# Kernel tuning notes

Measured on AMD Instinct MI355X. Metric: run time of the kernel, lower is better.

Reference implementation:

```python
import jax, jax.numpy as jnp
import numpy as np

B, T, IN = 512, 1024, 32
H, NL, DL, OUT = 128, 2, 256, 32


def _lstm_layer(xs, Wih, Whh, bih, bhh):
    # xs: [B, T, D]; Wih: [4H, D]; Whh: [4H, H]; biases: [4H]
    # PyTorch gate order: i, f, g, o
    x_gates = jnp.einsum('btd,gd->btg', xs, Wih) + bih + bhh  # [B,T,4H]

    def step(carry, xg):
        h, c = carry
        gates = xg + h @ Whh.T  # [B,4H]
        i, f, g, o = jnp.split(gates, 4, axis=-1)
        i = jax.nn.sigmoid(i)
        f = jax.nn.sigmoid(f)
        g = jnp.tanh(g)
        o = jax.nn.sigmoid(o)
        c = f * c + i * g
        h = o * jnp.tanh(c)
        return (h, c), h

    h0 = jnp.zeros((xs.shape[0], Whh.shape[1]), xs.dtype)
    c0 = jnp.zeros_like(h0)
    # scan over time axis
    (_, _), hs = jax.lax.scan(step, (h0, c0), jnp.swapaxes(x_gates, 0, 1))
    return jnp.swapaxes(hs, 0, 1)  # [B,T,H]


def setup_inputs() -> dict:
    key = jax.random.key(0)
    ks = jax.random.split(key, 16)
    s = 0.08  # ~1/sqrt(H)
    inp = {
        'x': jax.random.normal(ks[0], (B, T, IN), jnp.float32),
        'Wih0': jax.random.normal(ks[1], (4 * H, IN), jnp.float32) * s,
        'Whh0': jax.random.normal(ks[2], (4 * H, H), jnp.float32) * s,
        'bih0': jax.random.normal(ks[3], (4 * H,), jnp.float32) * s,
        'bhh0': jax.random.normal(ks[4], (4 * H,), jnp.float32) * s,
        'Wih1': jax.random.normal(ks[5], (4 * H, H), jnp.float32) * s,
        'Whh1': jax.random.normal(ks[6], (4 * H, H), jnp.float32) * s,
        'bih1': jax.random.normal(ks[7], (4 * H,), jnp.float32) * s,
        'bhh1': jax.random.normal(ks[8], (4 * H,), jnp.float32) * s,
        'W1': jax.random.normal(ks[9], (DL, H), jnp.float32) * s,
        'b1': jax.random.normal(ks[10], (DL,), jnp.float32) * s,
        'W2': jax.random.normal(ks[11], (OUT, DL), jnp.float32) * 0.06,
        'b2': jax.random.normal(ks[12], (OUT,), jnp.float32) * 0.06,
    }
    return inp


def reference(x, Wih0, Whh0, bih0, bhh0, Wih1, Whh1, bih1, bhh1, W1, b1, W2, b2):
    h = _lstm_layer(x, Wih0, Whh0, bih0, bhh0)
    h = _lstm_layer(h, Wih1, Whh1, bih1, bhh1)
    last = h[:, -1]  # [B,H]
    y = jax.nn.celu(last @ W1.T + b1)
    y = jax.nn.celu(y @ W2.T + b2)
    hidden_init = jnp.zeros((NL, x.shape[0], H), x.dtype)  # module returns its initial hidden
    return (y, hidden_init)
```

## Files before the change

### kernel.cpp

```cpp
#include <hip/hip_runtime.h>
#include <hip/hip_bf16.h>


#define DEV __device__ __forceinline__

typedef float f32x4 __attribute__((ext_vector_type(4)));
typedef short bf16x8 __attribute__((ext_vector_type(8)));
typedef unsigned short ushort_t;

DEV float sigm(float x) { return 1.f / (1.f + __expf(-x)); }
DEV float tanhfast(float x) { float e = __expf(2.f * x); return (e - 1.f) / (e + 1.f); }
DEV float celu1(float x) { return x > 0.f ? x : (__expf(x) - 1.f); }

DEV short f2bf(float f) {
    __hip_bfloat16 h = __float2bfloat16(f);
    return *reinterpret_cast<short*>(&h);
}

__global__ __launch_bounds__(256)
void cvt_bf16(const float* __restrict__ in, ushort_t* __restrict__ out, int n8)
{
    int i = blockIdx.x * 256 + threadIdx.x;
    if (i >= n8) return;
    const float4* p = (const float4*)(in + (size_t)i * 8);
    float4 a = p[0], b = p[1];
    bf16x8 v;
    v[0] = f2bf(a.x); v[1] = f2bf(a.y); v[2] = f2bf(a.z); v[3] = f2bf(a.w);
    v[4] = f2bf(b.x); v[5] = f2bf(b.y); v[6] = f2bf(b.z); v[7] = f2bf(b.w);
    *(bf16x8*)(out + (size_t)i * 8) = v;
}

template<int K, bool XMAP>
__global__ __launch_bounds__(256, 2)
void gemm_mfma(const ushort_t* __restrict__ A, const ushort_t* __restrict__ Wg,
               const float* __restrict__ bA, const float* __restrict__ bB,
               float* __restrict__ C, int t0, int TC)
{
    constexpr int SWB = K * 2;
    constexpr int SM  = (K == 32) ? 3 : 7;
    __shared__ char As[128 * SWB];
    __shared__ char Ws[128 * SWB];

    const int tid = threadIdx.x;
    const int r0 = blockIdx.x * 128;
    const int g0 = blockIdx.y * 128;
    const int lane = tid & 63, w = tid >> 6;
    const int lr = lane & 15, kg = lane >> 4;

    constexpr int UPR = SWB / 16;
    constexpr int NIT = 128 * UPR / 256;
#pragma unroll
    for (int e = 0; e < NIT; e++) {
        int idx = tid + e * 256;
        int row = idx / UPR;
        int kb  = (idx - row * UPR) * 16;
        int dst = row * SWB + (kb ^ ((row & SM) << 4));
        size_t src;
        int r = r0 + row;
        if (XMAP) {
            int b = r / TC, tt = r - b * TC;
            src = ((size_t)b * 1024 + (size_t)(t0 + tt)) * 32 + (size_t)(kb >> 1);
        } else {
            src = (size_t)r * K + (size_t)(kb >> 1);
        }
        *(bf16x8*)(As + dst) = *(const bf16x8*)(A + src);
        *(bf16x8*)(Ws + dst) = *(const bf16x8*)(Wg + (size_t)(g0 + row) * K + (size_t)(kb >> 1));
    }
    __syncthreads();

    f32x4 acc[2][8];
#pragma unroll
    for (int mi = 0; mi < 2; mi++)
#pragma unroll
        for (int n = 0; n < 8; n++) acc[mi][n] = (f32x4){0.f, 0.f, 0.f, 0.f};

    const int m0 = w * 32;
#pragma unroll
    for (int ks = 0; ks < K / 32; ks++) {
        const int kb = ks * 64 + kg * 16;
        const int ra0 = m0 + lr, ra1 = m0 + 16 + lr;
        bf16x8 a0 = *(const bf16x8*)(As + ra0 * SWB + (kb ^ ((ra0 & SM) << 4)));
        bf16x8 a1 = *(const bf16x8*)(As + ra1 * SWB + (kb ^ ((ra1 & SM) << 4)));
#pragma unroll
        for (int n = 0; n < 8; n++) {
            int wr = n * 16 + lr;
            bf16x8 bw = *(const bf16x8*)(Ws + wr * SWB + (kb ^ ((wr & SM) << 4)));
            acc[0][n] = __builtin_amdgcn_mfma_f32_16x16x32_bf16(a0, bw, acc[0][n], 0, 0, 0);
            acc[1][n] = __builtin_amdgcn_mfma_f32_16x16x32_bf16(a1, bw, acc[1][n], 0, 0, 0);
        }
    }

#pragma unroll
    for (int n = 0; n < 8; n++) {
        int g = g0 + n * 16 + lr;
        float bias = bA[g] + bB[g];
#pragma unroll
        for (int mi = 0; mi < 2; mi++) {
            int rrow = r0 + m0 + mi * 16 + kg * 4;
#pragma unroll
            for (int rr = 0; rr < 4; rr++)
                C[(size_t)(rrow + rr) * 512 + g] = acc[mi][n][rr] + bias;
        }
    }
}

template<int WRITE_H>
DEV void scan_body(const float* __restrict__ xg, const ushort_t* __restrict__ whh,
                   float* __restrict__ hs, float* __restrict__ cs,
                   ushort_t* __restrict__ hout, int TC, int blk)
{
    __shared__ short h_lds[16 * 128];
    __shared__ float pre[4 * 4 * 128];

    const int t    = threadIdx.x;
    const int lane = t & 63;
    const int w    = t >> 6;
    const int b0   = blk * 4;
    const int um   = t >> 7;
    const int uch  = t & 127;
    const int lr   = lane & 15, kg = lane >> 4;

    bf16x8 Wf[4][4];
#pragma unroll
    for (int q = 0; q < 4; q++)
#pragma unroll
        for (int kt = 0; kt < 4; kt++)
            Wf[q][kt] = *(const bf16x8*)(whh + (size_t)(q * 128 + w * 16 + lr) * 128
                                              + kt * 32 + kg * 8);
    asm volatile("" : "+v"(Wf[0][0]), "+v"(Wf[0][1]), "+v"(Wf[0][2]), "+v"(Wf[0][3]),
                      "+v"(Wf[1][0]), "+v"(Wf[1][1]), "+v"(Wf[1][2]), "+v"(Wf[1][3]),
                      "+v"(Wf[2][0]), "+v"(Wf[2][1]), "+v"(Wf[2][2]), "+v"(Wf[2][3]),
                      "+v"(Wf[3][0]), "+v"(Wf[3][1]), "+v"(Wf[3][2]), "+v"(Wf[3][3]));

    float c_reg  = cs[(size_t)(b0 + um) * 128 + uch];
    float h_keep = hs[(size_t)(b0 + um) * 128 + uch];
    *(short*)((char*)h_lds + um * 256 + ((uch * 2) ^ (um << 4))) = f2bf(h_keep);
    if (t < 384)
        *(unsigned long long*)((char*)h_lds + 4 * 256 + t * 8) = 0ull;
    __syncthreads();

    const int abase = lr * 256;
    const int aswz  = (lr & 7) << 4;
    const int akoff = kg * 16;

    for (int tt = 0; tt < TC; tt++) {
        const size_t xr = ((size_t)(b0 + um) * TC + tt) * 512 + uch;
        float xv0 = xg[xr];
        float xv1 = xg[xr + 128];
        float xv2 = xg[xr + 256];
        float xv3 = xg[xr + 384];

        bf16x8 Af[4];
#pragma unroll
        for (int kt = 0; kt < 4; kt++)
            Af[kt] = *(const bf16x8*)((const char*)h_lds + abase + ((kt * 64 + akoff) ^ aswz));

        f32x4 acc[4];
#pragma unroll
        for (int q = 0; q < 4; q++) {
            f32x4 a = {0.f, 0.f, 0.f, 0.f};
#pragma unroll
            for (int kt = 0; kt < 4; kt++)
                a = __builtin_amdgcn_mfma_f32_16x16x32_bf16(Af[kt], Wf[q][kt], a, 0, 0, 0);
            acc[q] = a;
        }

        if (kg == 0) {
            const int chw = w * 16 + lr;
#pragma unroll
            for (int q = 0; q < 4; q++)
#pragma unroll
                for (int r = 0; r < 4; r++)
                    pre[q * 512 + r * 128 + chw] = acc[q][r];
        }
        __syncthreads();

        float pi = pre[0 * 512 + um * 128 + uch] + xv0;
        float pf = pre[1 * 512 + um * 128 + uch] + xv1;
        float pg = pre[2 * 512 + um * 128 + uch] + xv2;
        float po = pre[3 * 512 + um * 128 + uch] + xv3;
        float iv = sigm(pi), fv = sigm(pf), gv = tanhfast(pg), ov = sigm(po);
        c_reg = fv * c_reg + iv * gv;
        float hv = ov * tanhfast(c_reg);
        h_keep = hv;
        short hb = f2bf(hv);
        *(short*)((char*)h_lds + um * 256 + ((uch * 2) ^ (um << 4))) = hb;
        if (WRITE_H)
            hout[((size_t)(b0 + um) * TC + tt) * 128 + uch] = (ushort_t)hb;
        __syncthreads();
    }

    hs[(size_t)(b0 + um) * 128 + uch] = h_keep;
    cs[(size_t)(b0 + um) * 128 + uch] = c_reg;
}

template<int WRITE_H>
__global__ __launch_bounds__(512, 2)
void lstm_scan(const float* __restrict__ xg, const ushort_t* __restrict__ whh,
               float* __restrict__ hs, float* __restrict__ cs,
               ushort_t* __restrict__ hout, int TC)
{
    scan_body<WRITE_H>(xg, whh, hs, cs, hout, TC, blockIdx.x);
}

__global__ __launch_bounds__(512, 2)
void lstm_scan_dual(const float* __restrict__ xg0, const ushort_t* __restrict__ whh0,
                    float* __restrict__ h0s, float* __restrict__ c0s,
                    ushort_t* __restrict__ hout,
                    const float* __restrict__ xg1, const ushort_t* __restrict__ whh1,
                    float* __restrict__ h1s, float* __restrict__ c1s, int TC)
{
    if (blockIdx.x < 128)
        scan_body<1>(xg0, whh0, h0s, c0s, hout, TC, blockIdx.x);
    else
        scan_body<0>(xg1, whh1, h1s, c1s, nullptr, TC, blockIdx.x - 128);
}

__global__ __launch_bounds__(256, 2)
void head_k(const float* __restrict__ h1s, const float* __restrict__ W1,
            const float* __restrict__ b1, const float* __restrict__ W2,
            const float* __restrict__ b2, float* __restrict__ out)
{
    __shared__ float hrow[128];
    __shared__ float y1[256];
    const int b = blockIdx.x;
    const int tid = threadIdx.x;
    if (tid < 128) hrow[tid] = h1s[(size_t)b * 128 + tid];
    __syncthreads();
    {
        float acc = b1[tid];
        const float4* wp = (const float4*)(W1 + (size_t)tid * 128);
        const float4* hp = (const float4*)hrow;
#pragma unroll 8
        for (int q = 0; q < 32; q++) {
            float4 wv = wp[q]; float4 hv = hp[q];
            acc += wv.x * hv.x + wv.y * hv.y + wv.z * hv.z + wv.w * hv.w;
        }
        y1[tid] = celu1(acc);
    }
    __syncthreads();
    if (tid < 32) {
        float acc = b2[tid];
        const float4* wp = (const float4*)(W2 + (size_t)tid * 256);
        const float4* yp = (const float4*)y1;
#pragma unroll 8
        for (int q = 0; q < 64; q++) {
            float4 wv = wp[q]; float4 yv = yp[q];
            acc += wv.x * yv.x + wv.y * yv.y + wv.z * yv.z + wv.w * yv.w;
        }
        out[(size_t)b * 32 + tid] = celu1(acc);
    }
}

extern "C" void kernel_launch(void* const* d_in, const int* in_sizes, int n_in,
                              void* d_out, int out_size, void* d_ws, size_t ws_size,
                              hipStream_t stream)
{
    const float* x    = (const float*)d_in[0];
    const float* Wih0 = (const float*)d_in[1];
    const float* Whh0 = (const float*)d_in[2];
    const float* bih0 = (const float*)d_in[3];
    const float* bhh0 = (const float*)d_in[4];
    const float* Wih1 = (const float*)d_in[5];
    const float* Whh1 = (const float*)d_in[6];
    const float* bih1 = (const float*)d_in[7];
    const float* bhh1 = (const float*)d_in[8];
    const float* W1   = (const float*)d_in[9];
    const float* b1   = (const float*)d_in[10];
    const float* W2   = (const float*)d_in[11];
    const float* b2   = (const float*)d_in[12];
    float* out = (float*)d_out;

    const size_t XN = 512ull * 1024 * 32;
    int TC = 128;
    while (TC > 8) {
        size_t need = (size_t)(2 * TC) * 512 * 512 * 4
                    + 4ull * 512 * 128 * 4
                    + ((size_t)512 * TC * 128 + XN + 512 * 32 + 3ull * 512 * 128) * 2;
        if (need <= ws_size) break;
        TC >>= 1;
    }

    float* xg0 = (float*)d_ws;
    float* xg1 = xg0 + (size_t)512 * TC * 512;
    float* st  = xg1 + (size_t)512 * TC * 512;
    float* h0s = st;
    float* c0s = st + 512 * 128;
    float* h1s = st + 2 * 512 * 128;
    float* c1s = st + 3 * 512 * 128;
    ushort_t* h0c  = (ushort_t*)(st + 4ull * 512 * 128);
    ushort_t* xbf  = h0c + (size_t)512 * TC * 128;
    ushort_t* wih0 = xbf + XN;
    ushort_t* wih1 = wih0 + 512 * 32;
    ushort_t* whh0 = wih1 + 512 * 128;
    ushort_t* whh1 = whh0 + 512 * 128;

    hipMemsetAsync(st, 0, (size_t)4 * 512 * 128 * 4, stream);
    hipMemsetAsync(out + 16384, 0, (size_t)131072 * 4, stream);

    cvt_bf16<<<(unsigned)(XN / 8 / 256), 256, 0, stream>>>(x, xbf, (int)(XN / 8));
    cvt_bf16<<<8,   256, 0, stream>>>(Wih0, wih0, 512 * 32 / 8);
    cvt_bf16<<<32,  256, 0, stream>>>(Wih1, wih1, 512 * 128 / 8);
    cvt_bf16<<<32,  256, 0, stream>>>(Whh0, whh0, 512 * 128 / 8);
    cvt_bf16<<<32,  256, 0, stream>>>(Whh1, whh1, 512 * 128 / 8);

    const int NC = 1024 / TC;
    dim3 ggrid((unsigned)(512 * TC / 128), 4);

    gemm_mfma<32, true ><<<ggrid, 256, 0, stream>>>(xbf, wih0, bih0, bhh0, xg0, 0, TC);
    lstm_scan<1><<<128, 512, 0, stream>>>(xg0, whh0, h0s, c0s, h0c, TC);
    for (int c = 1; c < NC; c++) {
        gemm_mfma<128, false><<<ggrid, 256, 0, stream>>>(h0c, wih1, bih1, bhh1, xg1, 0, TC);
        gemm_mfma<32,  true ><<<ggrid, 256, 0, stream>>>(xbf, wih0, bih0, bhh0, xg0, c * TC, TC);
        lstm_scan_dual<<<256, 512, 0, stream>>>(xg0, whh0, h0s, c0s, h0c,
                                                xg1, whh1, h1s, c1s, TC);
    }
    gemm_mfma<128, false><<<ggrid, 256, 0, stream>>>(h0c, wih1, bih1, bhh1, xg1, 0, TC);
    lstm_scan<0><<<128, 512, 0, stream>>>(xg1, whh1, h1s, c1s, nullptr, TC);

    head_k<<<512, 256, 0, stream>>>(h1s, W1, b1, W2, b2, out);
}
```

Measured before the change: 1.643 ms.

## Fuse bf16 conversion into GEMMs, store gate preacts in fp16, restructure scan step

Drops the separate fp32-to-bf16 conversion kernels and converts x and weights inside the GEMM tile loads and the scan prologue. The two per-chunk input-projection GEMMs are merged into one launch that selects its path by grid z. Precomputed gate inputs are stored as fp16 instead of fp32, halving that traffic. The scan step now applies gate activations directly from MFMA accumulators in the lanes that hold them, uses a double-buffered h tile in LDS so each step needs one barrier instead of two, and prefetches the next step's gate inputs into registers. The trade-offs are fp16 precision loss on gate preactivations, only 16 of 64 lanes per wave doing the elementwise work, and repeated conversion of x and weights on every GEMM tile.

```diff
diff --git a/kernel.cpp b/kernel.cpp
--- a/kernel.cpp
+++ b/kernel.cpp
@@ -1,5 +1,6 @@
 #include <hip/hip_runtime.h>
 #include <hip/hip_bf16.h>
+#include <hip/hip_fp16.h>
 
 
 #define DEV __device__ __forceinline__
@@ -16,34 +17,29 @@
     __hip_bfloat16 h = __float2bfloat16(f);
     return *reinterpret_cast<short*>(&h);
 }
-
-__global__ __launch_bounds__(256)
-void cvt_bf16(const float* __restrict__ in, ushort_t* __restrict__ out, int n8)
-{
-    int i = blockIdx.x * 256 + threadIdx.x;
-    if (i >= n8) return;
-    const float4* p = (const float4*)(in + (size_t)i * 8);
-    float4 a = p[0], b = p[1];
-    bf16x8 v;
-    v[0] = f2bf(a.x); v[1] = f2bf(a.y); v[2] = f2bf(a.z); v[3] = f2bf(a.w);
-    v[4] = f2bf(b.x); v[5] = f2bf(b.y); v[6] = f2bf(b.z); v[7] = f2bf(b.w);
-    *(bf16x8*)(out + (size_t)i * 8) = v;
+DEV ushort_t f2h(float f) {
+    __half h = __float2half(f);
+    return *reinterpret_cast<ushort_t*>(&h);
+}
+DEV float h2f(ushort_t u) {
+    __half h;
+    *reinterpret_cast<ushort_t*>(&h) = u;
+    return __half2float(h);
 }
 
 template<int K, bool XMAP>
-__global__ __launch_bounds__(256, 2)
-void gemm_mfma(const ushort_t* __restrict__ A, const ushort_t* __restrict__ Wg,
-               const float* __restrict__ bA, const float* __restrict__ bB,
-               float* __restrict__ C, int t0, int TC)
+DEV void gemm_body(char* lds, const void* Av, const float* __restrict__ Wg,
+                   const float* __restrict__ bA, const float* __restrict__ bB,
+                   ushort_t* __restrict__ C, int t0, int TC, int bx, int by)
 {
     constexpr int SWB = K * 2;
     constexpr int SM  = (K == 32) ? 3 : 7;
-    __shared__ char As[128 * SWB];
-    __shared__ char Ws[128 * SWB];
+    char* As = lds;
+    char* Ws = lds + 128 * SWB;
 
     const int tid = threadIdx.x;
-    const int r0 = blockIdx.x * 128;
-    const int g0 = blockIdx.y * 128;
+    const int r0 = bx * 128;
+    const int g0 = by * 128;
     const int lane = tid & 63, w = tid >> 6;
     const int lr = lane & 15, kg = lane >> 4;
 
@@ -55,16 +51,29 @@
         int row = idx / UPR;
         int kb  = (idx - row * UPR) * 16;
         int dst = row * SWB + (kb ^ ((row & SM) << 4));
-        size_t src;
-        int r = r0 + row;
+        int ke  = kb >> 1;
+        bf16x8 av;
         if (XMAP) {
+            const float* A = (const float*)Av;
+            int r = r0 + row;
             int b = r / TC, tt = r - b * TC;
-            src = ((size_t)b * 1024 + (size_t)(t0 + tt)) * 32 + (size_t)(kb >> 1);
+            const float* p = A + ((size_t)b * 1024 + (size_t)(t0 + tt)) * 32 + ke;
+            float4 f0 = *(const float4*)p, f1 = *(const float4*)(p + 4);
+            av[0] = f2bf(f0.x); av[1] = f2bf(f0.y); av[2] = f2bf(f0.z); av[3] = f2bf(f0.w);
+            av[4] = f2bf(f1.x); av[5] = f2bf(f1.y); av[6] = f2bf(f1.z); av[7] = f2bf(f1.w);
         } else {
-            src = (size_t)r * K + (size_t)(kb >> 1);
-        }
-        *(bf16x8*)(As + dst) = *(const bf16x8*)(A + src);
-        *(bf16x8*)(Ws + dst) = *(const bf16x8*)(Wg + (size_t)(g0 + row) * K + (size_t)(kb >> 1));
+            const ushort_t* A = (const ushort_t*)Av;
+            av = *(const bf16x8*)(A + (size_t)(r0 + row) * K + ke);
+        }
+        *(bf16x8*)(As + dst) = av;
+        {
+            const float* p = Wg + (size_t)(g0 + row) * K + ke;
+            float4 f0 = *(const float4*)p, f1 = *(const float4*)(p + 4);
+            bf16x8 wv;
+            wv[0] = f2bf(f0.x); wv[1] = f2bf(f0.y); wv[2] = f2bf(f0.z); wv[3] = f2bf(f0.w);
+            wv[4] = f2bf(f1.x); wv[5] = f2bf(f1.y); wv[6] = f2bf(f1.z); wv[7] = f2bf(f1.w);
+            *(bf16x8*)(Ws + dst) = wv;
+        }
     }
     __syncthreads();
 
@@ -99,62 +108,97 @@
             int rrow = r0 + m0 + mi * 16 + kg * 4;
 #pragma unroll
             for (int rr = 0; rr < 4; rr++)
-                C[(size_t)(rrow + rr) * 512 + g] = acc[mi][n][rr] + bias;
-        }
-    }
+                C[(size_t)(rrow + rr) * 512 + g] = f2h(acc[mi][n][rr] + bias);
+        }
+    }
+}
+
+template<int MODE>
+__global__ __launch_bounds__(256, 2)
+void gemm_pair(const float* __restrict__ x, const float* __restrict__ wih0,
+               const float* __restrict__ bih0, const float* __restrict__ bhh0,
+               ushort_t* __restrict__ xg0, int t0,
+               const ushort_t* __restrict__ h0c, const float* __restrict__ wih1,
+               const float* __restrict__ bih1, const float* __restrict__ bhh1,
+               ushort_t* __restrict__ xg1, int TC)
+{
+    __shared__ char lds[65536];
+    const int path = (MODE == 0) ? (int)blockIdx.z : ((MODE == 1) ? 0 : 1);
+    if (path == 0)
+        gemm_body<32,  true >(lds, x,   wih0, bih0, bhh0, xg0, t0, TC,
+                              blockIdx.x, blockIdx.y);
+    else
+        gemm_body<128, false>(lds, h0c, wih1, bih1, bhh1, xg1, 0, TC,
+                              blockIdx.x, blockIdx.y);
 }
 
 template<int WRITE_H>
-DEV void scan_body(const float* __restrict__ xg, const ushort_t* __restrict__ whh,
+DEV void scan_body(const ushort_t* __restrict__ xg, const float* __restrict__ whh,
                    float* __restrict__ hs, float* __restrict__ cs,
                    ushort_t* __restrict__ hout, int TC, int blk)
 {
-    __shared__ short h_lds[16 * 128];
-    __shared__ float pre[4 * 4 * 128];
+    __shared__ char hb[2][1024];
 
     const int t    = threadIdx.x;
     const int lane = t & 63;
     const int w    = t >> 6;
     const int b0   = blk * 4;
-    const int um   = t >> 7;
-    const int uch  = t & 127;
     const int lr   = lane & 15, kg = lane >> 4;
+    const int ch   = w * 16 + lr;
+    const int arow = lr & 3;
 
     bf16x8 Wf[4][4];
 #pragma unroll
     for (int q = 0; q < 4; q++)
 #pragma unroll
+        for (int kt = 0; kt < 4; kt++) {
+            const float* p = whh + (size_t)(q * 128 + ch) * 128 + kt * 32 + kg * 8;
+            bf16x8 v;
+#pragma unroll
+            for (int j = 0; j < 8; j++) v[j] = f2bf(p[j]);
+            Wf[q][kt] = v;
+        }
+
+    float cst[4] = {0.f, 0.f, 0.f, 0.f};
+    float hk[4]  = {0.f, 0.f, 0.f, 0.f};
+    if (lane < 16) {
+#pragma unroll
+        for (int r = 0; r < 4; r++) {
+            hk[r]  = hs[(size_t)(b0 + r) * 128 + ch];
+            cst[r] = cs[(size_t)(b0 + r) * 128 + ch];
+            *(short*)(&hb[0][0] + r * 256 + ((ch * 2) ^ (r << 6))) = f2bf(hk[r]);
+        }
+    }
+    __syncthreads();
+
+    ushort_t xpA[16], xpB[16];
+    if (lane < 16) {
+#pragma unroll
+        for (int r = 0; r < 4; r++)
+#pragma unroll
+            for (int q = 0; q < 4; q++)
+                xpA[r * 4 + q] = xg[(size_t)(b0 + r) * TC * 512 + q * 128 + ch];
+    }
+
+    auto step = [&](int tt, int rb, ushort_t (&xu)[16], ushort_t (&xl)[16], bool pre) {
+        asm volatile("" : "+v"(Wf[0][0]), "+v"(Wf[0][1]), "+v"(Wf[0][2]), "+v"(Wf[0][3]),
+                          "+v"(Wf[1][0]), "+v"(Wf[1][1]), "+v"(Wf[1][2]), "+v"(Wf[1][3]),
+                          "+v"(Wf[2][0]), "+v"(Wf[2][1]), "+v"(Wf[2][2]), "+v"(Wf[2][3]),
+                          "+v"(Wf[3][0]), "+v"(Wf[3][1]), "+v"(Wf[3][2]), "+v"(Wf[3][3]));
+        const char* hbase = hb[rb];
+        bf16x8 Af[4];
+#pragma unroll
         for (int kt = 0; kt < 4; kt++)
-            Wf[q][kt] = *(const bf16x8*)(whh + (size_t)(q * 128 + w * 16 + lr) * 128
-                                              + kt * 32 + kg * 8);
-    asm volatile("" : "+v"(Wf[0][0]), "+v"(Wf[0][1]), "+v"(Wf[0][2]), "+v"(Wf[0][3]),
-                      "+v"(Wf[1][0]), "+v"(Wf[1][1]), "+v"(Wf[1][2]), "+v"(Wf[1][3]),
-                      "+v"(Wf[2][0]), "+v"(Wf[2][1]), "+v"(Wf[2][2]), "+v"(Wf[2][3]),
-                      "+v"(Wf[3][0]), "+v"(Wf[3][1]), "+v"(Wf[3][2]), "+v"(Wf[3][3]));
-
-    float c_reg  = cs[(size_t)(b0 + um) * 128 + uch];
-    float h_keep = hs[(size_t)(b0 + um) * 128 + uch];
-    *(short*)((char*)h_lds + um * 256 + ((uch * 2) ^ (um << 4))) = f2bf(h_keep);
-    if (t < 384)
-        *(unsigned long long*)((char*)h_lds + 4 * 256 + t * 8) = 0ull;
-    __syncthreads();
-
-    const int abase = lr * 256;
-    const int aswz  = (lr & 7) << 4;
-    const int akoff = kg * 16;
-
-    for (int tt = 0; tt < TC; tt++) {
-        const size_t xr = ((size_t)(b0 + um) * TC + tt) * 512 + uch;
-        float xv0 = xg[xr];
-        float xv1 = xg[xr + 128];
-        float xv2 = xg[xr + 256];
-        float xv3 = xg[xr + 384];
-
-        bf16x8 Af[4];
-#pragma unroll
-        for (int kt = 0; kt < 4; kt++)
-            Af[kt] = *(const bf16x8*)((const char*)h_lds + abase + ((kt * 64 + akoff) ^ aswz));
-
+            Af[kt] = *(const bf16x8*)(hbase + arow * 256
+                                      + ((kt * 64 + kg * 16) ^ (arow << 6)));
+        if (pre && lane < 16) {
+#pragma unroll
+            for (int r = 0; r < 4; r++)
+#pragma unroll
+                for (int q = 0; q < 4; q++)
+                    xl[r * 4 + q] = xg[((size_t)(b0 + r) * TC + (tt + 1)) * 512
+                                       + q * 128 + ch];
+        }
         f32x4 acc[4];
 #pragma unroll
         for (int q = 0; q < 4; q++) {
@@ -164,39 +208,44 @@
                 a = __builtin_amdgcn_mfma_f32_16x16x32_bf16(Af[kt], Wf[q][kt], a, 0, 0, 0);
             acc[q] = a;
         }
-
-        if (kg == 0) {
-            const int chw = w * 16 + lr;
-#pragma unroll
-            for (int q = 0; q < 4; q++)
-#pragma unroll
-                for (int r = 0; r < 4; r++)
-                    pre[q * 512 + r * 128 + chw] = acc[q][r];
+        if (lane < 16) {
+            char* hw = hb[rb ^ 1];
+#pragma unroll
+            for (int r = 0; r < 4; r++) {
+                float pi = acc[0][r] + h2f(xu[r * 4 + 0]);
+                float pf = acc[1][r] + h2f(xu[r * 4 + 1]);
+                float pg = acc[2][r] + h2f(xu[r * 4 + 2]);
+                float po = acc[3][r] + h2f(xu[r * 4 + 3]);
+                float iv = sigm(pi), fv = sigm(pf), gv = tanhfast(pg), ov = sigm(po);
+                cst[r] = fv * cst[r] + iv * gv;
+                float hv = ov * tanhfast(cst[r]);
+                hk[r] = hv;
+                short hb16 = f2bf(hv);
+                *(short*)(hw + r * 256 + ((ch * 2) ^ (r << 6))) = hb16;
+                if (WRITE_H)
+                    hout[((size_t)(b0 + r) * TC + tt) * 128 + ch] = (ushort_t)hb16;
+            }
         }
         __syncthreads();
-
-        float pi = pre[0 * 512 + um * 128 + uch] + xv0;
-        float pf = pre[1 * 512 + um * 128 + uch] + xv1;
-        float pg = pre[2 * 512 + um * 128 + uch] + xv2;
-        float po = pre[3 * 512 + um * 128 + uch] + xv3;
-        float iv = sigm(pi), fv = sigm(pf), gv = tanhfast(pg), ov = sigm(po);
-        c_reg = fv * c_reg + iv * gv;
-        float hv = ov * tanhfast(c_reg);
-        h_keep = hv;
-        short hb = f2bf(hv);
-        *(short*)((char*)h_lds + um * 256 + ((uch * 2) ^ (um << 4))) = hb;
-        if (WRITE_H)
-            hout[((size_t)(b0 + um) * TC + tt) * 128 + uch] = (ushort_t)hb;
-        __syncthreads();
-    }
-
-    hs[(size_t)(b0 + um) * 128 + uch] = h_keep;
-    cs[(size_t)(b0 + um) * 128 + uch] = c_reg;
+    };
+
+    for (int tt = 0; tt < TC; tt += 2) {
+        step(tt,     0, xpA, xpB, true);
+        step(tt + 1, 1, xpB, xpA, (tt + 2) < TC);
+    }
+
+    if (lane < 16) {
+#pragma unroll
+        for (int r = 0; r < 4; r++) {
+            hs[(size_t)(b0 + r) * 128 + ch] = hk[r];
+            cs[(size_t)(b0 + r) * 128 + ch] = cst[r];
+        }
+    }
 }
 
 template<int WRITE_H>
 __global__ __launch_bounds__(512, 2)
-void lstm_scan(const float* __restrict__ xg, const ushort_t* __restrict__ whh,
+void lstm_scan(const ushort_t* __restrict__ xg, const float* __restrict__ whh,
                float* __restrict__ hs, float* __restrict__ cs,
                ushort_t* __restrict__ hout, int TC)
 {
@@ -204,10 +253,10 @@
 }
 
 __global__ __launch_bounds__(512, 2)
-void lstm_scan_dual(const float* __restrict__ xg0, const ushort_t* __restrict__ whh0,
+void lstm_scan_dual(const ushort_t* __restrict__ xg0, const float* __restrict__ whh0,
                     float* __restrict__ h0s, float* __restrict__ c0s,
                     ushort_t* __restrict__ hout,
-                    const float* __restrict__ xg1, const ushort_t* __restrict__ whh1,
+                    const ushort_t* __restrict__ xg1, const float* __restrict__ whh1,
                     float* __restrict__ h1s, float* __restrict__ c1s, int TC)
 {
     if (blockIdx.x < 128)
@@ -271,52 +320,42 @@
     const float* b2   = (const float*)d_in[12];
     float* out = (float*)d_out;
 
-    const size_t XN = 512ull * 1024 * 32;
     int TC = 128;
     while (TC > 8) {
-        size_t need = (size_t)(2 * TC) * 512 * 512 * 4
-                    + 4ull * 512 * 128 * 4
-                    + ((size_t)512 * TC * 128 + XN + 512 * 32 + 3ull * 512 * 128) * 2;
+        size_t need = 2ull * 512 * TC * 512 * 2 + (size_t)512 * TC * 128 * 2
+                    + 4ull * 512 * 128 * 4;
         if (need <= ws_size) break;
         TC >>= 1;
     }
 
-    float* xg0 = (float*)d_ws;
-    float* xg1 = xg0 + (size_t)512 * TC * 512;
-    float* st  = xg1 + (size_t)512 * TC * 512;
+    ushort_t* xg0 = (ushort_t*)d_ws;
+    ushort_t* xg1 = xg0 + (size_t)512 * TC * 512;
+    ushort_t* h0c = xg1 + (size_t)512 * TC * 512;
+    float* st  = (float*)(h0c + (size_t)512 * TC * 128);
     float* h0s = st;
     float* c0s = st + 512 * 128;
     float* h1s = st + 2 * 512 * 128;
     float* c1s = st + 3 * 512 * 128;
-    ushort_t* h0c  = (ushort_t*)(st + 4ull * 512 * 128);
-    ushort_t* xbf  = h0c + (size_t)512 * TC * 128;
-    ushort_t* wih0 = xbf + XN;
-    ushort_t* wih1 = wih0 + 512 * 32;
-    ushort_t* whh0 = wih1 + 512 * 128;
-    ushort_t* whh1 = whh0 + 512 * 128;
 
     hipMemsetAsync(st, 0, (size_t)4 * 512 * 128 * 4, stream);
     hipMemsetAsync(out + 16384, 0, (size_t)131072 * 4, stream);
 
-    cvt_bf16<<<(unsigned)(XN / 8 / 256), 256, 0, stream>>>(x, xbf, (int)(XN / 8));
-    cvt_bf16<<<8,   256, 0, stream>>>(Wih0, wih0, 512 * 32 / 8);
-    cvt_bf16<<<32,  256, 0, stream>>>(Wih1, wih1, 512 * 128 / 8);
-    cvt_bf16<<<32,  256, 0, stream>>>(Whh0, whh0, 512 * 128 / 8);
-    cvt_bf16<<<32,  256, 0, stream>>>(Whh1, whh1, 512 * 128 / 8);
-
     const int NC = 1024 / TC;
-    dim3 ggrid((unsigned)(512 * TC / 128), 4);
-
-    gemm_mfma<32, true ><<<ggrid, 256, 0, stream>>>(xbf, wih0, bih0, bhh0, xg0, 0, TC);
-    lstm_scan<1><<<128, 512, 0, stream>>>(xg0, whh0, h0s, c0s, h0c, TC);
+    dim3 g1((unsigned)(512 * TC / 128), 4, 1);
+    dim3 g2((unsigned)(512 * TC / 128), 4, 2);
+
+    gemm_pair<1><<<g1, 256, 0, stream>>>(x, Wih0, bih0, bhh0, xg0, 0,
+                                         nullptr, Wih1, bih1, bhh1, xg1, TC);
+    lstm_scan<1><<<128, 512, 0, stream>>>(xg0, Whh0, h0s, c0s, h0c, TC);
     for (int c = 1; c < NC; c++) {
-        gemm_mfma<128, false><<<ggrid, 256, 0, stream>>>(h0c, wih1, bih1, bhh1, xg1, 0, TC);
-        gemm_mfma<32,  true ><<<ggrid, 256, 0, stream>>>(xbf, wih0, bih0, bhh0, xg0, c * TC, TC);
-        lstm_scan_dual<<<256, 512, 0, stream>>>(xg0, whh0, h0s, c0s, h0c,
-                                                xg1, whh1, h1s, c1s, TC);
-    }
-    gemm_mfma<128, false><<<ggrid, 256, 0, stream>>>(h0c, wih1, bih1, bhh1, xg1, 0, TC);
-    lstm_scan<0><<<128, 512, 0, stream>>>(xg1, whh1, h1s, c1s, nullptr, TC);
+        gemm_pair<0><<<g2, 256, 0, stream>>>(x, Wih0, bih0, bhh0, xg0, c * TC,
+                                             h0c, Wih1, bih1, bhh1, xg1, TC);
+        lstm_scan_dual<<<256, 512, 0, stream>>>(xg0, Whh0, h0s, c0s, h0c,
+                                                xg1, Whh1, h1s, c1s, TC);
+    }
+    gemm_pair<2><<<g1, 256, 0, stream>>>(x, Wih0, bih0, bhh0, xg0, 0,
+                                         h0c, Wih1, bih1, bhh1, xg1, TC);
+    lstm_scan<0><<<128, 512, 0, stream>>>(xg1, Whh1, h1s, c1s, nullptr, TC);
 
     head_k<<<512, 256, 0, stream>>>(h1s, W1, b1, W2, b2, out);
 }
```

Result: slower. 2.669 ms (+62.5%).
